# Kernel tuning notes

Measured on AMD Instinct MI355X. Metric: run time of the kernel, lower is better.

Reference implementation:

```python
import jax, jax.numpy as jnp
import numpy as np

H_DIM = 2048
N_HEADS = 16

def setup_inputs() -> dict:
    key = jax.random.key(0)
    ks = jax.random.split(key, 9)
    B, T, C = 2, 2048, H_DIM
    scale = 1.0 / np.sqrt(C)  # lecun_normal approx
    src = jax.random.normal(ks[0], (B, T, C), dtype=jnp.float32)
    Wq = jax.random.normal(ks[1], (C, H_DIM), dtype=jnp.float32) * scale
    Wk = jax.random.normal(ks[2], (C, H_DIM), dtype=jnp.float32) * scale
    Wv = jax.random.normal(ks[3], (C, H_DIM), dtype=jnp.float32) * scale
    Wo = jax.random.normal(ks[4], (H_DIM, H_DIM), dtype=jnp.float32) * scale
    bq = jnp.zeros((H_DIM,), jnp.float32)
    bk = jnp.zeros((H_DIM,), jnp.float32)
    bv = jnp.zeros((H_DIM,), jnp.float32)
    bo = jnp.zeros((H_DIM,), jnp.float32)
    return {"src": src, "Wq": Wq, "bq": bq, "Wk": Wk, "bk": bk,
            "Wv": Wv, "bv": bv, "Wo": Wo, "bo": bo}

def reference(src, Wq, bq, Wk, bk, Wv, bv, Wo, bo):
    B, T, C = src.shape
    N = N_HEADS
    D = C // N
    def heads(x):  # [B,T,h_dim] -> [B,N,T,D]
        return x.reshape(B, T, N, D).transpose(0, 2, 1, 3)
    q = heads(src @ Wq + bq)
    k = heads(src @ Wk + bk)
    v = heads(src @ Wv + bv)
    # scaled dot-product with causal mask
    scores = jnp.einsum('bntd,bnsd->bnts', q, k) / jnp.sqrt(jnp.float32(D))
    causal = jnp.tril(jnp.ones((T, T), dtype=bool))
    scores = jnp.where(causal[None, None], scores, -jnp.inf)
    attn = jax.nn.softmax(scores, axis=-1)
    out = jnp.einsum('bnts,bnsd->bntd', attn, v)  # dropout is identity (drop_p=0)
    out = out.transpose(0, 2, 1, 3).reshape(B, T, N * D)
    return out @ Wo + bo
```

## Files before the change

kernel.cpp:

```cpp
#include <hip/hip_runtime.h>
#include <hip/hip_bf16.h>

typedef float f32x4 __attribute__((ext_vector_type(4)));
typedef __bf16 bf16x8v __attribute__((ext_vector_type(8)));
typedef __bf16 bf16x4v __attribute__((ext_vector_type(4)));
typedef unsigned uint2v __attribute__((ext_vector_type(2)));
typedef bf16x8v __attribute__((may_alias)) bf16x8;
typedef bf16x4v __attribute__((may_alias)) bf16x4;
typedef uint2v __attribute__((may_alias)) u32x2;

typedef __attribute__((address_space(1))) const void gvoid_t;
typedef __attribute__((address_space(3))) void lvoid_t;

#define DEVINL __device__ __forceinline__

#define BDIM 2
#define TDIM 2048
#define CDIM 2048
#define NHEAD 16
#define DHEAD 128
#define MROWS 4096
#define WSZ ((size_t)CDIM * CDIM)
#define XSZ ((size_t)MROWS * CDIM)

#define BARRIER_LGKM() asm volatile("s_waitcnt lgkmcnt(0)\ns_barrier" ::: "memory")

DEVINL __bf16 f2bf(float f) {
  unsigned u = __builtin_bit_cast(unsigned, f);
  u += 0x7fffu + ((u >> 16) & 1u);
  unsigned short h = (unsigned short)(u >> 16);
  return __builtin_bit_cast(__bf16, h);
}

DEVINL unsigned pk2bf_trunc(float lo, float hi) {
  return __builtin_amdgcn_perm(__builtin_bit_cast(unsigned, hi),
                               __builtin_bit_cast(unsigned, lo), 0x07060302);
}

DEVINL void gl2lds16(const void* g, void* l) {
  __builtin_amdgcn_global_load_lds((gvoid_t*)g, (lvoid_t*)l, 16, 0, 0);
}

__global__ void detect_dtype(const unsigned* __restrict__ w,
                             int* __restrict__ flag, int* __restrict__ cnt) {
  const int l = threadIdx.x;
  if (l == 0) *cnt = 0;
  const unsigned word = w[l];
  const unsigned e = (word >> 7) & 0xFFu;
  const int vote = (e >= 0x70u && e <= 0x87u) ? 1 : 0;
  const unsigned long long m = __ballot(vote);
  if (l == 0) *flag = (__popcll(m) >= 32) ? 1 : 0;
}

__global__ __launch_bounds__(256) void cvt_src(const void* __restrict__ in,
                                               __bf16* __restrict__ out,
                                               const int* __restrict__ flag,
                                               int n8) {
  const int i = blockIdx.x * 256 + threadIdx.x;
  if (i >= n8) return;
  if (*flag) {
    ((bf16x8*)out)[i] = ((const bf16x8*)in)[i];
  } else {
    const float* f = (const float*)in + (size_t)i * 8;
    bf16x8v v;
#pragma unroll
    for (int j = 0; j < 8; ++j) v[j] = f2bf(f[j]);
    ((bf16x8*)out)[i] = v;
  }
}

__global__ __launch_bounds__(256) void cvt_wt(
    const void* __restrict__ w0, const void* __restrict__ w1,
    const void* __restrict__ w2, const void* __restrict__ w3,
    __bf16* __restrict__ out, const int* __restrict__ flag) {
  __shared__ __attribute__((aligned(16))) __bf16 tile[64][68];
  const void* W = (blockIdx.z == 0) ? w0 : (blockIdx.z == 1) ? w1
                : (blockIdx.z == 2) ? w2 : w3;
  __bf16* Wt = out + (size_t)blockIdx.z * WSZ;
  const int tx = threadIdx.x & 63, ty = threadIdx.x >> 6;
  const int k0 = blockIdx.x * 64, n0 = blockIdx.y * 64;
  const int fl = *flag;
#pragma unroll
  for (int i = ty; i < 64; i += 4) {
    const size_t off = (size_t)(k0 + i) * CDIM + n0 + tx;
    const float v = fl ? (float)((const __bf16*)W)[off] : ((const float*)W)[off];
    tile[i][tx] = f2bf(v);
  }
  __syncthreads();
#pragma unroll
  for (int i = ty; i < 64; i += 4)
    Wt[(size_t)(n0 + i) * CDIM + k0 + tx] = tile[tx][i];
}

__global__ __launch_bounds__(256) void cvt_bias(
    const void* __restrict__ b0, const void* __restrict__ b1,
    const void* __restrict__ b2, const void* __restrict__ b3,
    float* __restrict__ out, const int* __restrict__ flag) {
  const int i = blockIdx.x * 256 + threadIdx.x;
  const void* b = (i < 2048) ? b0 : (i < 4096) ? b1 : (i < 6144) ? b2 : b3;
  const int idx = i & 2047;
  out[i] = (*flag) ? (float)((const __bf16*)b)[idx] : ((const float*)b)[idx];
}

template <int NTN, int MODE>
__global__ __launch_bounds__(512, 2) void gemm256(
    const __bf16* __restrict__ A, const __bf16* __restrict__ Bt,
    const float* __restrict__ bias, __bf16* __restrict__ qb,
    __bf16* __restrict__ kb, __bf16* __restrict__ vtb,
    const int* __restrict__ flag, void* __restrict__ outp) {
  constexpr int K = CDIM;
  constexpr int NKT = K / 64;
  __shared__ __attribute__((aligned(16))) __bf16 Als[2][256 * 64];
  __shared__ __attribute__((aligned(16))) __bf16 Bls[2][256 * 64];

  const int tid = threadIdx.x;
  const int w = tid >> 6, l = tid & 63;
  const int quad = l >> 4, l16 = l & 15;
  const int wm = w >> 2, wn = w & 3;

  const int bid = blockIdx.x;
  const int bm = bid & 15, bn = bid >> 4;
  const int m0 = bm * 256, n0 = bn * 256;

  const int srow = tid >> 3;
  const int scb = (tid & 7) ^ (srow & 7);
  const __bf16* gA = A + (size_t)(m0 + srow) * K + scb * 8;
  const __bf16* gB = Bt + (size_t)(n0 + srow) * K + scb * 8;
  const int wl = w * 512;

  int cp[2];
  cp[0] = ((0 + quad) ^ (l16 & 7)) * 8;
  cp[1] = ((4 + quad) ^ (l16 & 7)) * 8;

  f32x4 acc[8][4];
#pragma unroll
  for (int i = 0; i < 8; ++i)
#pragma unroll
    for (int j = 0; j < 4; ++j) acc[i][j] = (f32x4){0.f, 0.f, 0.f, 0.f};

#pragma unroll
  for (int u = 0; u < 4; ++u)
    gl2lds16(gA + (size_t)u * 64 * K, &Als[0][u * 4096 + wl]);
#pragma unroll
  for (int u = 0; u < 4; ++u)
    gl2lds16(gB + (size_t)u * 64 * K, &Bls[0][u * 4096 + wl]);

#define PHASE(MH, KS, DO_B, S0, S1)                                           \
  {                                                                           \
    if (DO_B) {                                                               \
      _Pragma("unroll") for (int nf = 0; nf < 4; ++nf)                        \
          bfr[nf] = *(const bf16x8*)&Bb[(wn * 64 + nf * 16 + l16) * 64 +      \
                                        cp[KS]];                              \
    }                                                                         \
    bf16x8 afr[4];                                                            \
    _Pragma("unroll") for (int i = 0; i < 4; ++i)                             \
        afr[i] = *(const bf16x8*)&Ab[(wm * 128 + (MH) * 64 + i * 16 + l16) *  \
                                         64 +                                 \
                                     cp[KS]];                                 \
    if (kt + 1 < NKT) {                                                       \
      S0;                                                                     \
      S1;                                                                     \
    }                                                                         \
    __builtin_amdgcn_s_barrier();                                             \
    asm volatile("s_waitcnt lgkmcnt(0)" ::: "memory");                        \
    __builtin_amdgcn_sched_barrier(0);                                        \
    __builtin_amdgcn_s_setprio(1);                                            \
    _Pragma("unroll") for (int i = 0; i < 4; ++i)                             \
        _Pragma("unroll") for (int nf = 0; nf < 4; ++nf)                      \
            acc[(MH) * 4 + i][nf] = __builtin_amdgcn_mfma_f32_16x16x32_bf16(  \
                afr[i], bfr[nf], acc[(MH) * 4 + i][nf], 0, 0, 0);             \
    __builtin_amdgcn_s_setprio(0);                                            \
    __builtin_amdgcn_s_barrier();                                             \
  }

  for (int kt = 0; kt < NKT; ++kt) {
    asm volatile("s_waitcnt vmcnt(0)" ::: "memory");
    __builtin_amdgcn_sched_barrier(0);
    __builtin_amdgcn_s_barrier();

    const __bf16* Ab = Als[kt & 1];
    const __bf16* Bb = Bls[kt & 1];
    const int nb = (kt + 1) & 1;
    const size_t ko = (size_t)(kt + 1) * 64;
    bf16x8 bfr[4];

    PHASE(0, 0, 1,
          gl2lds16(gA + ko, &Als[nb][wl]),
          gl2lds16(gA + (size_t)64 * K + ko, &Als[nb][4096 + wl]))
    PHASE(1, 0, 0,
          gl2lds16(gA + (size_t)128 * K + ko, &Als[nb][8192 + wl]),
          gl2lds16(gA + (size_t)192 * K + ko, &Als[nb][12288 + wl]))
    PHASE(0, 1, 1,
          gl2lds16(gB + ko, &Bls[nb][wl]),
          gl2lds16(gB + (size_t)64 * K + ko, &Bls[nb][4096 + wl]))
    PHASE(1, 1, 0,
          gl2lds16(gB + (size_t)128 * K + ko, &Bls[nb][8192 + wl]),
          gl2lds16(gB + (size_t)192 * K + ko, &Bls[nb][12288 + wl]))
  }
#undef PHASE

  if (MODE == 0) {
    const int mat = n0 >> 11;
#pragma unroll
    for (int nf = 0; nf < 4; ++nf) {
      const int n = n0 + wn * 64 + nf * 16 + l16;
      const int nn = n & 2047;
      const int h = nn >> 7, d = nn & 127;
      const float bv = bias[n];
#pragma unroll
      for (int mi = 0; mi < 8; ++mi) {
        const int mbase = m0 + wm * 128 + mi * 16 + quad * 4;
        const int bb = mbase >> 11, t = mbase & 2047;
        if (mat == 2) {
          bf16x4v v4;
#pragma unroll
          for (int r = 0; r < 4; ++r) v4[r] = f2bf(acc[mi][nf][r] + bv);
          *(bf16x4*)&vtb[((size_t)(bb * NHEAD + h) * DHEAD + d) * TDIM + t] = v4;
        } else {
          __bf16* op = (mat == 0) ? qb : kb;
#pragma unroll
          for (int r = 0; r < 4; ++r)
            op[((size_t)(bb * NHEAD + h) * TDIM + t + r) * DHEAD + d] =
                f2bf(acc[mi][nf][r] + bv);
        }
      }
    }
  } else {
    const int ofl = *flag;
#pragma unroll
    for (int nf = 0; nf < 4; ++nf) {
      const int n = n0 + wn * 64 + nf * 16 + l16;
      const float bv = bias[n];
#pragma unroll
      for (int mi = 0; mi < 8; ++mi) {
#pragma unroll
        for (int r = 0; r < 4; ++r) {
          const int m = m0 + wm * 128 + mi * 16 + quad * 4 + r;
          const float v = acc[mi][nf][r] + bv;
          if (ofl) ((__bf16*)outp)[(size_t)m * CDIM + n] = f2bf(v);
          else     ((float*)outp)[(size_t)m * CDIM + n] = v;
        }
      }
    }
  }
}

__global__ __launch_bounds__(256, 2) void attn(
    const __bf16* __restrict__ Q, const __bf16* __restrict__ K,
    const __bf16* __restrict__ Vt, __bf16* __restrict__ ctx,
    int* __restrict__ cnt) {
  constexpr float CSC = 0.12753139726f;
  __shared__ __attribute__((aligned(16))) __bf16 Kls[64 * 128];
  __shared__ __attribute__((aligned(16))) __bf16 Vls[128 * 64];
  __shared__ __attribute__((aligned(16))) __bf16 Pls[4][32 * 64];
  __shared__ int jobLds;

  const int tid = threadIdx.x;
  const int w = tid >> 6, l = tid & 63, quad = l >> 4, l16 = l & 15;

  const int krow = tid >> 4;
  const int kcol = tid & 15;
  const int kldsoff = ((kcol ^ krow) * 8);
  const int vrow = tid >> 3;
  const int vcol = tid & 7;
  const int vldsoff = ((vcol ^ (vrow & 7)) * 8);

  for (;;) {
    __syncthreads();
    if (tid == 0) jobLds = atomicAdd(cnt, 1);
    __syncthreads();
    const int j = jobLds;
    if (j >= 512) break;
    const int qt = 15 - (j >> 5);
    const int bh = j & 31;
    const int t0w = qt * 128 + w * 32;
    const __bf16* Qbh = Q + (size_t)bh * TDIM * DHEAD;
    const __bf16* Kbh = K + (size_t)bh * TDIM * DHEAD;
    const __bf16* Vbh = Vt + (size_t)bh * TDIM * DHEAD;

    bf16x8 qf[2][4];
#pragma unroll
    for (int tt = 0; tt < 2; ++tt)
#pragma unroll
      for (int ks = 0; ks < 4; ++ks)
        qf[tt][ks] = *(const bf16x8*)(Qbh +
                     (size_t)(t0w + tt * 16 + l16) * DHEAD + ks * 32 + quad * 8);

    f32x4 oacc[8][2];
#pragma unroll
    for (int dt = 0; dt < 8; ++dt)
#pragma unroll
      for (int tt = 0; tt < 2; ++tt) oacc[dt][tt] = (f32x4){0.f, 0.f, 0.f, 0.f};
    float mrow[2] = {-1e30f, -1e30f};
    float lrow[2] = {0.f, 0.f};

    const int nsb = 2 * (qt + 1);

    bf16x8 kr[4], vr[4];
#pragma unroll
    for (int p = 0; p < 4; ++p)
      kr[p] = *(const bf16x8*)(Kbh + (size_t)(p * 16 + krow) * DHEAD + kcol * 8);
#pragma unroll
    for (int p = 0; p < 4; ++p)
      vr[p] = *(const bf16x8*)(Vbh + (size_t)(p * 32 + vrow) * TDIM + vcol * 8);

    for (int sb = 0; sb < nsb; ++sb) {
      const int s0 = sb * 64;
      BARRIER_LGKM();
#pragma unroll
      for (int p = 0; p < 4; ++p)
        *(bf16x8*)&Kls[(p * 16 + krow) * 128 + kldsoff] = kr[p];
#pragma unroll
      for (int p = 0; p < 4; ++p)
        *(bf16x8*)&Vls[(p * 32 + vrow) * 64 + vldsoff] = vr[p];
      if (sb + 1 < nsb) {
        const int s1 = s0 + 64;
#pragma unroll
        for (int p = 0; p < 4; ++p)
          kr[p] = *(const bf16x8*)(Kbh + (size_t)(s1 + p * 16 + krow) * DHEAD +
                                   kcol * 8);
#pragma unroll
        for (int p = 0; p < 4; ++p)
          vr[p] = *(const bf16x8*)(Vbh + (size_t)(p * 32 + vrow) * TDIM + s1 +
                                   vcol * 8);
      }
      BARRIER_LGKM();
      if (s0 > t0w + 31) continue;

      f32x4 sacc[4][2];
#pragma unroll
      for (int st = 0; st < 4; ++st)
#pragma unroll
        for (int tt = 0; tt < 2; ++tt) sacc[st][tt] = (f32x4){0.f, 0.f, 0.f, 0.f};
#pragma unroll
      for (int ks = 0; ks < 4; ++ks) {
        bf16x8 kf[4];
#pragma unroll
        for (int st = 0; st < 4; ++st)
          kf[st] = *(const bf16x8*)&Kls[(st * 16 + l16) * 128 +
                                        (((ks * 4 + quad) ^ l16) * 8)];
#pragma unroll
        for (int st = 0; st < 4; ++st)
#pragma unroll
          for (int tt = 0; tt < 2; ++tt)
            sacc[st][tt] = __builtin_amdgcn_mfma_f32_16x16x32_bf16(
                kf[st], qf[tt][ks], sacc[st][tt], 0, 0, 0);
      }
      if (s0 + 63 > t0w) {
#pragma unroll
        for (int st = 0; st < 4; ++st)
#pragma unroll
          for (int tt = 0; tt < 2; ++tt)
#pragma unroll
            for (int r = 0; r < 4; ++r) {
              const int s = s0 + st * 16 + quad * 4 + r;
              const int t = t0w + tt * 16 + l16;
              if (s > t) sacc[st][tt][r] = -1e30f;
            }
      }
#pragma unroll
      for (int tt = 0; tt < 2; ++tt) {
        float vm = -1e30f;
#pragma unroll
        for (int st = 0; st < 4; ++st)
#pragma unroll
          for (int r = 0; r < 4; ++r) vm = fmaxf(vm, sacc[st][tt][r]);
        vm = fmaxf(vm, __shfl_xor(vm, 16));
        vm = fmaxf(vm, __shfl_xor(vm, 32));
        const float mnew = fmaxf(mrow[tt], vm);
        if (__ballot(mnew > mrow[tt])) {
          const float alpha = exp2f((mrow[tt] - mnew) * CSC);
          lrow[tt] *= alpha;
#pragma unroll
          for (int dt = 0; dt < 8; ++dt)
#pragma unroll
            for (int r = 0; r < 4; ++r) oacc[dt][tt][r] *= alpha;
          mrow[tt] = mnew;
        }
        float rs = 0.f;
#pragma unroll
        for (int st = 0; st < 4; ++st) {
          const float p0 = exp2f((sacc[st][tt][0] - mnew) * CSC);
          const float p1 = exp2f((sacc[st][tt][1] - mnew) * CSC);
          const float p2 = exp2f((sacc[st][tt][2] - mnew) * CSC);
          const float p3 = exp2f((sacc[st][tt][3] - mnew) * CSC);
          rs += (p0 + p1) + (p2 + p3);
          u32x2 pk = {pk2bf_trunc(p0, p1), pk2bf_trunc(p2, p3)};
          *(u32x2*)&Pls[w][(tt * 16 + l16) * 64 +
                           (((st * 2 + (quad >> 1)) ^ (l16 & 7)) * 8) +
                           (quad & 1) * 4] = pk;
        }
        rs += __shfl_xor(rs, 16);
        rs += __shfl_xor(rs, 32);
        lrow[tt] += rs;
      }
      asm volatile("s_waitcnt lgkmcnt(0)" ::: "memory");
#pragma unroll
      for (int ks = 0; ks < 2; ++ks) {
        bf16x8 pf[2];
#pragma unroll
        for (int tt = 0; tt < 2; ++tt)
          pf[tt] = *(const bf16x8*)&Pls[w][(tt * 16 + l16) * 64 +
                                           (((ks * 4 + quad) ^ (l16 & 7)) * 8)];
#pragma unroll
        for (int dt = 0; dt < 8; ++dt) {
          const bf16x8 vf =
              *(const bf16x8*)&Vls[(dt * 16 + l16) * 64 +
                                   (((ks * 4 + quad) ^ (l16 & 7)) * 8)];
#pragma unroll
          for (int tt = 0; tt < 2; ++tt)
            oacc[dt][tt] = __builtin_amdgcn_mfma_f32_16x16x32_bf16(
                vf, pf[tt], oacc[dt][tt], 0, 0, 0);
        }
      }
    }

    const int b = bh >> 4, h = bh & 15;
#pragma unroll
    for (int tt = 0; tt < 2; ++tt) {
      const float rinv = 1.0f / lrow[tt];
      const int t = t0w + tt * 16 + l16;
      __bf16* cp = ctx + ((size_t)(b * TDIM + t)) * CDIM + h * DHEAD;
#pragma unroll
      for (int dt = 0; dt < 8; ++dt) {
        bf16x4v v4;
#pragma unroll
        for (int r = 0; r < 4; ++r) v4[r] = f2bf(oacc[dt][tt][r] * rinv);
        *(bf16x4*)&cp[dt * 16 + quad * 4] = v4;
      }
    }
  }
}

extern "C" void kernel_launch(void* const* d_in, const int* in_sizes, int n_in,
                              void* d_out, int out_size, void* d_ws,
                              size_t ws_size, hipStream_t stream) {
  const void* src = d_in[0];
  const void* Wq = d_in[1];
  const void* bq = d_in[2];
  const void* Wk = d_in[3];
  const void* bk = d_in[4];
  const void* Wv = d_in[5];
  const void* bv = d_in[6];
  const void* Wo = d_in[7];
  const void* bo = d_in[8];

  char* wsb = (char*)d_ws;
  int* flag = (int*)wsb;
  int* cnt = (int*)(wsb + 128);
  __bf16* srcbf = (__bf16*)(wsb + 256);
  __bf16* wqt = srcbf + XSZ;
  __bf16* wkt = wqt + WSZ;
  __bf16* wvt = wkt + WSZ;
  __bf16* wot = wvt + WSZ;
  __bf16* qb = wot + WSZ;
  __bf16* kb = qb + XSZ;
  __bf16* vtb = kb + XSZ;
  float* biasf = (float*)(vtb + XSZ);
  __bf16* ctx = srcbf;

  detect_dtype<<<1, 64, 0, stream>>>((const unsigned*)src, flag, cnt);
  cvt_src<<<4096, 256, 0, stream>>>(src, srcbf, flag, (int)(XSZ / 8));
  cvt_wt<<<dim3(32, 32, 4), 256, 0, stream>>>(Wq, Wk, Wv, Wo, wqt, flag);
  cvt_bias<<<32, 256, 0, stream>>>(bq, bk, bv, bo, biasf, flag);
  gemm256<24, 0><<<384, 512, 0, stream>>>(srcbf, wqt, biasf, qb, kb, vtb,
                                          nullptr, nullptr);
  attn<<<512, 256, 0, stream>>>(qb, kb, vtb, ctx, cnt);
  gemm256<8, 1><<<128, 512, 0, stream>>>(ctx, wot, biasf + 6144, nullptr,
                                         nullptr, nullptr, flag, d_out);
}
```

Measured before the change: 441.1 us.

## Replace GEMM with 128x256 tiles and a 4-stage half-K LDS ring pipeline

Both projection GEMMs shrink their tile from 256x256 to 128x256 and now stream K in 32-wide half-steps through a 4-slot LDS ring with three stages in flight, using vmcnt-based waits instead of a full drain each step. Doubling the grid (768 and 256 blocks) is meant to fill more of the CUs on MI355X, and the deeper prefetch is meant to hide global-to-LDS latency. In exchange, each tile reuses less data, so global traffic per FLOP rises, and the hand-written vmcnt and barrier sequencing becomes harder to get right.

```diff
diff --git a/kernel.cpp b/kernel.cpp
--- a/kernel.cpp
+++ b/kernel.cpp
@@ -102,16 +102,16 @@
   out[i] = (*flag) ? (float)((const __bf16*)b)[idx] : ((const float*)b)[idx];
 }
 
-template <int NTN, int MODE>
-__global__ __launch_bounds__(512, 2) void gemm256(
+template <int MODE>
+__global__ __launch_bounds__(512, 2) void gemmring(
     const __bf16* __restrict__ A, const __bf16* __restrict__ Bt,
     const float* __restrict__ bias, __bf16* __restrict__ qb,
     __bf16* __restrict__ kb, __bf16* __restrict__ vtb,
     const int* __restrict__ flag, void* __restrict__ outp) {
   constexpr int K = CDIM;
   constexpr int NKT = K / 64;
-  __shared__ __attribute__((aligned(16))) __bf16 Als[2][256 * 64];
-  __shared__ __attribute__((aligned(16))) __bf16 Bls[2][256 * 64];
+  __shared__ __attribute__((aligned(16))) __bf16 Asl[4][128 * 32];
+  __shared__ __attribute__((aligned(16))) __bf16 Bsl[4][256 * 32];
 
   const int tid = threadIdx.x;
   const int w = tid >> 6, l = tid & 63;
@@ -119,85 +119,111 @@
   const int wm = w >> 2, wn = w & 3;
 
   const int bid = blockIdx.x;
-  const int bm = bid & 15, bn = bid >> 4;
-  const int m0 = bm * 256, n0 = bn * 256;
-
-  const int srow = tid >> 3;
-  const int scb = (tid & 7) ^ (srow & 7);
-  const __bf16* gA = A + (size_t)(m0 + srow) * K + scb * 8;
-  const __bf16* gB = Bt + (size_t)(n0 + srow) * K + scb * 8;
-  const int wl = w * 512;
-
-  int cp[2];
-  cp[0] = ((0 + quad) ^ (l16 & 7)) * 8;
-  cp[1] = ((4 + quad) ^ (l16 & 7)) * 8;
-
-  f32x4 acc[8][4];
-#pragma unroll
-  for (int i = 0; i < 8; ++i)
+  const int bm = bid & 31, bn = bid >> 5;
+  const int m0 = bm * 128, n0 = bn * 256;
+
+  const int ls = (tid & 7) ^ ((tid >> 3) & 7);
+  const int rbase = 2 * (tid >> 3) + (ls >> 2);
+  const int cb8 = (ls & 3) * 8;
+  const __bf16* gAh = A + (size_t)(m0 + rbase) * K + cb8;
+  const __bf16* gBh = Bt + (size_t)(n0 + rbase) * K + cb8;
+
+  const int L2 = l16 >> 1;
+  const int physr = (((l16 & 1) << 2) + quad) ^ L2;
+  const int lane_e = L2 * 64 + physr * 8;
+
+#define STAGE_A(h)                                                       \
+  gl2lds16(gAh + (size_t)(((h) >> 1) * 64 + ((h) & 1) * 32),             \
+           (__bf16*)Asl[(h) & 3] + w * 512)
+#define STAGE_B(h, e)                                                    \
+  gl2lds16(gBh + (size_t)(e) * 128 * K +                                 \
+               (((h) >> 1) * 64 + ((h) & 1) * 32),                       \
+           (__bf16*)Bsl[(h) & 3] + (e) * 4096 + w * 512)
+
+  f32x4 acc[4][4];
+#pragma unroll
+  for (int i = 0; i < 4; ++i)
 #pragma unroll
     for (int j = 0; j < 4; ++j) acc[i][j] = (f32x4){0.f, 0.f, 0.f, 0.f};
 
-#pragma unroll
-  for (int u = 0; u < 4; ++u)
-    gl2lds16(gA + (size_t)u * 64 * K, &Als[0][u * 4096 + wl]);
-#pragma unroll
-  for (int u = 0; u < 4; ++u)
-    gl2lds16(gB + (size_t)u * 64 * K, &Bls[0][u * 4096 + wl]);
-
-#define PHASE(MH, KS, DO_B, S0, S1)                                           \
-  {                                                                           \
-    if (DO_B) {                                                               \
-      _Pragma("unroll") for (int nf = 0; nf < 4; ++nf)                        \
-          bfr[nf] = *(const bf16x8*)&Bb[(wn * 64 + nf * 16 + l16) * 64 +      \
-                                        cp[KS]];                              \
-    }                                                                         \
-    bf16x8 afr[4];                                                            \
-    _Pragma("unroll") for (int i = 0; i < 4; ++i)                             \
-        afr[i] = *(const bf16x8*)&Ab[(wm * 128 + (MH) * 64 + i * 16 + l16) *  \
-                                         64 +                                 \
-                                     cp[KS]];                                 \
-    if (kt + 1 < NKT) {                                                       \
-      S0;                                                                     \
-      S1;                                                                     \
-    }                                                                         \
-    __builtin_amdgcn_s_barrier();                                             \
-    asm volatile("s_waitcnt lgkmcnt(0)" ::: "memory");                        \
-    __builtin_amdgcn_sched_barrier(0);                                        \
-    __builtin_amdgcn_s_setprio(1);                                            \
-    _Pragma("unroll") for (int i = 0; i < 4; ++i)                             \
-        _Pragma("unroll") for (int nf = 0; nf < 4; ++nf)                      \
-            acc[(MH) * 4 + i][nf] = __builtin_amdgcn_mfma_f32_16x16x32_bf16(  \
-                afr[i], bfr[nf], acc[(MH) * 4 + i][nf], 0, 0, 0);             \
-    __builtin_amdgcn_s_setprio(0);                                            \
-    __builtin_amdgcn_s_barrier();                                             \
-  }
+  STAGE_A(0); STAGE_B(0, 0); STAGE_B(0, 1);
+  STAGE_A(1); STAGE_B(1, 0); STAGE_B(1, 1);
+  STAGE_A(2); STAGE_B(2, 0); STAGE_B(2, 1);
+  asm volatile("s_waitcnt vmcnt(6)" ::: "memory");
+  __builtin_amdgcn_sched_barrier(0);
+  __builtin_amdgcn_s_barrier();
+
+#define MFMA8(NF0)                                                        \
+  __builtin_amdgcn_s_setprio(1);                                          \
+  _Pragma("unroll") for (int mi = 0; mi < 4; ++mi) {                      \
+    acc[mi][(NF0)] = __builtin_amdgcn_mfma_f32_16x16x32_bf16(             \
+        afr[mi], bfr[0], acc[mi][(NF0)], 0, 0, 0);                        \
+    acc[mi][(NF0) + 1] = __builtin_amdgcn_mfma_f32_16x16x32_bf16(         \
+        afr[mi], bfr[1], acc[mi][(NF0) + 1], 0, 0, 0);                    \
+  }                                                                       \
+  __builtin_amdgcn_s_setprio(0);
+
+#define LGKM_BAR()                                                        \
+  __builtin_amdgcn_s_barrier();                                           \
+  asm volatile("s_waitcnt lgkmcnt(0)" ::: "memory");                      \
+  __builtin_amdgcn_sched_barrier(0)
 
   for (int kt = 0; kt < NKT; ++kt) {
-    asm volatile("s_waitcnt vmcnt(0)" ::: "memory");
+    const int h0 = 2 * kt;
+    const __bf16* Ab0 = Asl[h0 & 3];
+    const __bf16* Bb0 = Bsl[h0 & 3];
+    const __bf16* Ab1 = Asl[(h0 + 1) & 3];
+    const __bf16* Bb1 = Bsl[(h0 + 1) & 3];
+    bf16x8 afr[4], bfr[2];
+
+#pragma unroll
+    for (int mi = 0; mi < 4; ++mi)
+      afr[mi] = *(const bf16x8*)&Ab0[(wm * 64 + mi * 16) * 32 + lane_e];
+    bfr[0] = *(const bf16x8*)&Bb0[(wn * 64 + 0 * 16) * 32 + lane_e];
+    bfr[1] = *(const bf16x8*)&Bb0[(wn * 64 + 1 * 16) * 32 + lane_e];
+    if (kt <= NKT - 2) { STAGE_A(h0 + 3); STAGE_B(h0 + 3, 0); }
+    LGKM_BAR();
+    MFMA8(0)
+    __builtin_amdgcn_s_barrier();
+
+    bfr[0] = *(const bf16x8*)&Bb0[(wn * 64 + 2 * 16) * 32 + lane_e];
+    bfr[1] = *(const bf16x8*)&Bb0[(wn * 64 + 3 * 16) * 32 + lane_e];
+    if (kt <= NKT - 2) { STAGE_B(h0 + 3, 1); }
+    LGKM_BAR();
+    MFMA8(2)
+    if (kt < NKT - 1)
+      asm volatile("s_waitcnt vmcnt(6)" ::: "memory");
+    else
+      asm volatile("s_waitcnt vmcnt(0)" ::: "memory");
     __builtin_amdgcn_sched_barrier(0);
     __builtin_amdgcn_s_barrier();
 
-    const __bf16* Ab = Als[kt & 1];
-    const __bf16* Bb = Bls[kt & 1];
-    const int nb = (kt + 1) & 1;
-    const size_t ko = (size_t)(kt + 1) * 64;
-    bf16x8 bfr[4];
-
-    PHASE(0, 0, 1,
-          gl2lds16(gA + ko, &Als[nb][wl]),
-          gl2lds16(gA + (size_t)64 * K + ko, &Als[nb][4096 + wl]))
-    PHASE(1, 0, 0,
-          gl2lds16(gA + (size_t)128 * K + ko, &Als[nb][8192 + wl]),
-          gl2lds16(gA + (size_t)192 * K + ko, &Als[nb][12288 + wl]))
-    PHASE(0, 1, 1,
-          gl2lds16(gB + ko, &Bls[nb][wl]),
-          gl2lds16(gB + (size_t)64 * K + ko, &Bls[nb][4096 + wl]))
-    PHASE(1, 1, 0,
-          gl2lds16(gB + (size_t)128 * K + ko, &Bls[nb][8192 + wl]),
-          gl2lds16(gB + (size_t)192 * K + ko, &Bls[nb][12288 + wl]))
+#pragma unroll
+    for (int mi = 0; mi < 4; ++mi)
+      afr[mi] = *(const bf16x8*)&Ab1[(wm * 64 + mi * 16) * 32 + lane_e];
+    bfr[0] = *(const bf16x8*)&Bb1[(wn * 64 + 0 * 16) * 32 + lane_e];
+    bfr[1] = *(const bf16x8*)&Bb1[(wn * 64 + 1 * 16) * 32 + lane_e];
+    if (kt <= NKT - 3) { STAGE_A(h0 + 4); STAGE_B(h0 + 4, 0); }
+    LGKM_BAR();
+    MFMA8(0)
+    __builtin_amdgcn_s_barrier();
+
+    bfr[0] = *(const bf16x8*)&Bb1[(wn * 64 + 2 * 16) * 32 + lane_e];
+    bfr[1] = *(const bf16x8*)&Bb1[(wn * 64 + 3 * 16) * 32 + lane_e];
+    if (kt <= NKT - 3) { STAGE_B(h0 + 4, 1); }
+    LGKM_BAR();
+    MFMA8(2)
+    if (kt < NKT - 2)
+      asm volatile("s_waitcnt vmcnt(6)" ::: "memory");
+    else if (kt == NKT - 2)
+      asm volatile("s_waitcnt vmcnt(3)" ::: "memory");
+    __builtin_amdgcn_sched_barrier(0);
+    __builtin_amdgcn_s_barrier();
   }
-#undef PHASE
+#undef MFMA8
+#undef LGKM_BAR
+#undef STAGE_A
+#undef STAGE_B
 
   if (MODE == 0) {
     const int mat = n0 >> 11;
@@ -208,8 +234,8 @@
       const int h = nn >> 7, d = nn & 127;
       const float bv = bias[n];
 #pragma unroll
-      for (int mi = 0; mi < 8; ++mi) {
-        const int mbase = m0 + wm * 128 + mi * 16 + quad * 4;
+      for (int mi = 0; mi < 4; ++mi) {
+        const int mbase = m0 + wm * 64 + mi * 16 + quad * 4;
         const int bb = mbase >> 11, t = mbase & 2047;
         if (mat == 2) {
           bf16x4v v4;
@@ -232,10 +258,10 @@
       const int n = n0 + wn * 64 + nf * 16 + l16;
       const float bv = bias[n];
 #pragma unroll
-      for (int mi = 0; mi < 8; ++mi) {
+      for (int mi = 0; mi < 4; ++mi) {
 #pragma unroll
         for (int r = 0; r < 4; ++r) {
-          const int m = m0 + wm * 128 + mi * 16 + quad * 4 + r;
+          const int m = m0 + wm * 64 + mi * 16 + quad * 4 + r;
           const float v = acc[mi][nf][r] + bv;
           if (ofl) ((__bf16*)outp)[(size_t)m * CDIM + n] = f2bf(v);
           else     ((float*)outp)[(size_t)m * CDIM + n] = v;
@@ -463,9 +489,9 @@
   cvt_src<<<4096, 256, 0, stream>>>(src, srcbf, flag, (int)(XSZ / 8));
   cvt_wt<<<dim3(32, 32, 4), 256, 0, stream>>>(Wq, Wk, Wv, Wo, wqt, flag);
   cvt_bias<<<32, 256, 0, stream>>>(bq, bk, bv, bo, biasf, flag);
-  gemm256<24, 0><<<384, 512, 0, stream>>>(srcbf, wqt, biasf, qb, kb, vtb,
-                                          nullptr, nullptr);
+  gemmring<0><<<768, 512, 0, stream>>>(srcbf, wqt, biasf, qb, kb, vtb,
+                                       nullptr, nullptr);
   attn<<<512, 256, 0, stream>>>(qb, kb, vtb, ctx, cnt);
-  gemm256<8, 1><<<128, 512, 0, stream>>>(ctx, wot, biasf + 6144, nullptr,
-                                         nullptr, nullptr, flag, d_out);
-}
+  gemmring<1><<<256, 512, 0, stream>>>(ctx, wot, biasf + 6144, nullptr,
+                                       nullptr, nullptr, flag, d_out);
+}
```

New measurement: 426.6 us. 3.3% less time.
